# Optimization experiments

Measured on AMD Instinct MI355X. Metric: run time of the kernel, lower is better.

The kernel has to match this reference:

```python
import jax, jax.numpy as jnp
import numpy as np

N_NODES = 32  # nodes per topological level
H = 256       # hidden size
D_IN = 64     # edge feature dim
T, E = 512, 128


def _lstm_layer(x, src, dst, Wih, Whh, b, reverse):
    """One direction of one layer over the layered lattice.
    x: [T,E,Din], src/dst: [T,E] node ids in [0,N_NODES).
    Returns per-edge hidden [T,E,H].
    """
    if reverse:  # traverse lattice in reverse topological order
        x = x[::-1]
        s, d = dst[::-1], src[::-1]
    else:
        s, d = src, dst
    h0 = jnp.zeros((N_NODES, H), x.dtype)
    c0 = jnp.zeros((N_NODES, H), x.dtype)

    def step(carry, inp):
        hn, cn = carry
        xe, se, de = inp
        hs, cs = hn[se], cn[se]                      # gather source-node states [E,H]
        gates = xe @ Wih.T + hs @ Whh.T + b          # LSTMCell: [E,4H]
        i, f, g, o = jnp.split(gates, 4, axis=-1)
        c = jax.nn.sigmoid(f) * cs + jax.nn.sigmoid(i) * jnp.tanh(g)
        h = jax.nn.sigmoid(o) * jnp.tanh(c)
        # combine_edges('mean'): segment-mean of incoming edges per dest node
        cnt = jax.ops.segment_sum(jnp.ones((E,), x.dtype), de, num_segments=N_NODES)
        denom = jnp.maximum(cnt, 1.0)[:, None]
        hn2 = jax.ops.segment_sum(h, de, num_segments=N_NODES) / denom
        cn2 = jax.ops.segment_sum(c, de, num_segments=N_NODES) / denom
        return (hn2, cn2), h

    _, eh = jax.lax.scan(step, (h0, c0), (x, s, d))
    if reverse:
        eh = eh[::-1]
    return eh


def setup_inputs() -> dict:
    key = jax.random.key(0)
    ks = jax.random.split(key, 16)
    x = jax.random.normal(ks[0], (T, E, D_IN), jnp.float32)
    src = jax.random.randint(ks[1], (T, E), 0, N_NODES, jnp.int32)
    dst = jax.random.randint(ks[2], (T, E), 0, N_NODES, jnp.int32)
    sc = 1.0 / np.sqrt(H)
    u = lambda k, shp: jax.random.uniform(k, shp, jnp.float32, -sc, sc)
    # layer 0: input D_IN; layer 1: input 2H (bidirectional concat). dim 0 = direction
    W_ih0 = u(ks[3], (2, 4 * H, D_IN))
    W_hh0 = u(ks[4], (2, 4 * H, H))
    b0 = u(ks[5], (2, 4 * H))
    W_ih1 = u(ks[6], (2, 4 * H, 2 * H))
    W_hh1 = u(ks[7], (2, 4 * H, H))
    b1 = u(ks[8], (2, 4 * H))
    return {"x": x, "W_ih0": W_ih0, "W_hh0": W_hh0, "b0": b0,
            "W_ih1": W_ih1, "W_hh1": W_hh1, "b1": b1,
            "src": src, "dst": dst}


def reference(x, W_ih0, W_hh0, b0, W_ih1, W_hh1, b1, src, dst):
    out = x
    for Wih, Whh, b in ((W_ih0, W_hh0, b0), (W_ih1, W_hh1, b1)):
        fwd = _lstm_layer(out, src, dst, Wih[0], Whh[0], b[0], reverse=False)
        bwd = _lstm_layer(out, src, dst, Wih[1], Whh[1], b[1], reverse=True)
        out = jnp.concatenate([fwd, bwd], axis=-1)  # [T,E,2H]
    return out
```

## Files before the change

### kernel.cpp

```cpp
#include <hip/hip_runtime.h>

#define T_STEPS 512
#define E_EDGES 128
#define NN 32
#define HH 256
#define G4 1024
#define NWG 64
#define TPB 256

typedef __attribute__((ext_vector_type(8))) short s8v;
typedef __attribute__((ext_vector_type(4))) float f4v;
typedef unsigned long long u64;

__device__ __forceinline__ float fsig(float x) {
  x = fminf(fmaxf(x, -30.f), 30.f);
  return 1.f / (1.f + __expf(-x));
}
__device__ __forceinline__ float ftanh(float x) {
  float xc = fminf(fmaxf(x, -15.f), 15.f);
  float e = __expf(2.f * xc);
  return (e - 1.f) / (e + 1.f);
}
__device__ __forceinline__ float b2f(short s) {
  return __uint_as_float(((unsigned)(unsigned short)s) << 16);
}
__device__ __forceinline__ void bar_lds() {
  asm volatile("s_waitcnt lgkmcnt(0)\n\ts_barrier" ::: "memory");
}

__global__ __launch_bounds__(128) void prep_kernel(const int* __restrict__ src,
    const int* __restrict__ dst, int* __restrict__ eord, int* __restrict__ eoff) {
  __shared__ int de0[E_EDGES], de1[E_EDGES], off0[NN + 1], off1[NN + 1];
  const int t = blockIdx.x, e = threadIdx.x;
  de0[e] = dst[t * E_EDGES + e];
  de1[e] = src[t * E_EDGES + e];
  __syncthreads();
  if (e == 0) {
    int c[NN];
    for (int i = 0; i < NN; ++i) c[i] = 0;
    for (int i = 0; i < E_EDGES; ++i) c[de0[i]]++;
    int s = 0;
    for (int i = 0; i < NN; ++i) { off0[i] = s; s += c[i]; }
    off0[NN] = E_EDGES;
  }
  if (e == 1) {
    int c[NN];
    for (int i = 0; i < NN; ++i) c[i] = 0;
    for (int i = 0; i < E_EDGES; ++i) c[de1[i]]++;
    int s = 0;
    for (int i = 0; i < NN; ++i) { off1[i] = s; s += c[i]; }
    off1[NN] = E_EDGES;
  }
  __syncthreads();
  int d0 = de0[e], r0 = 0, d1 = de1[e], r1 = 0;
  for (int i = 0; i < e; ++i) {
    r0 += (de0[i] == d0);
    r1 += (de1[i] == d1);
  }
  eord[((size_t)0 * T_STEPS + t) * E_EDGES + off0[d0] + r0] = e;
  eord[((size_t)1 * T_STEPS + (T_STEPS - 1 - t)) * E_EDGES + off1[d1] + r1] = e;
  if (e < NN + 1) {
    eoff[((size_t)0 * T_STEPS + t) * (NN + 1) + e] = off0[e];
    eoff[((size_t)1 * T_STEPS + (T_STEPS - 1 - t)) * (NN + 1) + e] = off1[e];
  }
}

template <int M>
__global__ __launch_bounds__(256) void gates_mfma(
    const float* __restrict__ In, const float* __restrict__ W,
    const float* __restrict__ b, float* __restrict__ Gx, int reverse, int t0,
    int Cs) {
  __shared__ short WsT[2][128][72];
  __shared__ short XsT[2][128][72];
  __shared__ float biasL[128];
  const int tid = threadIdx.x;
  const int kb = blockIdx.x;
  const int lt = blockIdx.y;
  const int t = t0 + lt;
  const int tsrc = reverse ? (T_STEPS - 1 - t) : t;
  const float* Inb = In + (size_t)tsrc * E_EDGES * M;

  if (tid < 128) biasL[tid] = b[kb * 128 + tid];

  const int lane = tid & 63, wv = tid >> 6;
  const int ll = lane & 15, lh = lane >> 4;
  const int srow = tid >> 1, sh32 = (tid & 1) * 32;

  f4v acc[2][8];
#pragma unroll
  for (int i = 0; i < 2; ++i)
#pragma unroll
    for (int j = 0; j < 8; ++j) acc[i][j] = (f4v){0.f, 0.f, 0.f, 0.f};

  for (int mc = 0; mc < M; mc += 64) {
    __syncthreads();
    {
      const float* wr = W + (size_t)(kb * 128 + srow) * M + mc + sh32;
      const float* xr = Inb + (size_t)srow * M + mc + sh32;
#pragma unroll
      for (int i = 0; i < 8; ++i) {
        float4 a = *(const float4*)(wr + i * 4);
        float4 x = *(const float4*)(xr + i * 4);
        unsigned ua[4] = {__float_as_uint(a.x), __float_as_uint(a.y),
                          __float_as_uint(a.z), __float_as_uint(a.w)};
        unsigned ux[4] = {__float_as_uint(x.x), __float_as_uint(x.y),
                          __float_as_uint(x.z), __float_as_uint(x.w)};
        unsigned la[4], lx[4];
#pragma unroll
        for (int u = 0; u < 4; ++u) {
          la[u] = __float_as_uint(__uint_as_float(ua[u]) -
                                  __uint_as_float(ua[u] & 0xFFFF0000u));
          lx[u] = __float_as_uint(__uint_as_float(ux[u]) -
                                  __uint_as_float(ux[u] & 0xFFFF0000u));
        }
        int off = sh32 + i * 4;
        *(unsigned*)&WsT[0][srow][off + 0] = (ua[0] >> 16) | (ua[1] & 0xFFFF0000u);
        *(unsigned*)&WsT[0][srow][off + 2] = (ua[2] >> 16) | (ua[3] & 0xFFFF0000u);
        *(unsigned*)&WsT[1][srow][off + 0] = (la[0] >> 16) | (la[1] & 0xFFFF0000u);
        *(unsigned*)&WsT[1][srow][off + 2] = (la[2] >> 16) | (la[3] & 0xFFFF0000u);
        *(unsigned*)&XsT[0][srow][off + 0] = (ux[0] >> 16) | (ux[1] & 0xFFFF0000u);
        *(unsigned*)&XsT[0][srow][off + 2] = (ux[2] >> 16) | (ux[3] & 0xFFFF0000u);
        *(unsigned*)&XsT[1][srow][off + 0] = (lx[0] >> 16) | (lx[1] & 0xFFFF0000u);
        *(unsigned*)&XsT[1][srow][off + 2] = (lx[2] >> 16) | (lx[3] & 0xFFFF0000u);
      }
    }
    __syncthreads();
#pragma unroll
    for (int ks = 0; ks < 2; ++ks) {
      const int mo = ks * 32 + lh * 8;
      s8v ah0 = *(const s8v*)&WsT[0][wv * 32 + ll][mo];
      s8v al0 = *(const s8v*)&WsT[1][wv * 32 + ll][mo];
      s8v ah1 = *(const s8v*)&WsT[0][wv * 32 + 16 + ll][mo];
      s8v al1 = *(const s8v*)&WsT[1][wv * 32 + 16 + ll][mo];
#pragma unroll
      for (int et = 0; et < 8; ++et) {
        s8v bh = *(const s8v*)&XsT[0][et * 16 + ll][mo];
        s8v blo = *(const s8v*)&XsT[1][et * 16 + ll][mo];
        acc[0][et] = __builtin_amdgcn_mfma_f32_16x16x32_bf16(ah0, bh, acc[0][et], 0, 0, 0);
        acc[0][et] = __builtin_amdgcn_mfma_f32_16x16x32_bf16(ah0, blo, acc[0][et], 0, 0, 0);
        acc[0][et] = __builtin_amdgcn_mfma_f32_16x16x32_bf16(al0, bh, acc[0][et], 0, 0, 0);
        acc[1][et] = __builtin_amdgcn_mfma_f32_16x16x32_bf16(ah1, bh, acc[1][et], 0, 0, 0);
        acc[1][et] = __builtin_amdgcn_mfma_f32_16x16x32_bf16(ah1, blo, acc[1][et], 0, 0, 0);
        acc[1][et] = __builtin_amdgcn_mfma_f32_16x16x32_bf16(al1, bh, acc[1][et], 0, 0, 0);
      }
    }
  }
#pragma unroll
  for (int kt = 0; kt < 2; ++kt) {
    const int kloc = wv * 32 + kt * 16 + lh * 4;
    const int kg = kb * 128 + kloc;
    const int gate = kg >> 8;
    const int ch = kg & 255;
    const int slot = ch >> 3;
    const int jj0 = ch & 7;
    const float4 bv = *(const float4*)&biasL[kloc];
    float* gb = Gx + ((((size_t)slot * Cs + lt) * 4 + gate) * E_EDGES) * 8 + jj0;
#pragma unroll
    for (int et = 0; et < 8; ++et) {
      int e = et * 16 + ll;
      f4v v = acc[kt][et];
      *(float4*)(gb + (size_t)e * 8) =
          make_float4(v[0] + bv.x, v[1] + bv.y, v[2] + bv.z, v[3] + bv.w);
    }
  }
}

__global__ __launch_bounds__(TPB) void recur_kernel(
    const float* __restrict__ GxF, const float* __restrict__ GxB,
    const float* __restrict__ WhhF, const float* __restrict__ WhhB,
    const int* __restrict__ src, const int* __restrict__ dst,
    const int* __restrict__ eord, const int* __restrict__ eoff,
    u64* hnG, float* cnG, float* outBase,
    int t0, int nsteps) {
  __shared__ short WsB[2][32][33][8];
  __shared__ short hnB[2][32][33][8];
  __shared__ float zF[32][33];
  __shared__ float hE[E_EDGES][8];
  __shared__ float cE[E_EDGES][8];
  __shared__ float cnL[NN][9];
  __shared__ int eordL[E_EDGES];
  __shared__ int eoffL[NN + 1];
  __shared__ int mfmaOK;

  const int tid = threadIdx.x;
  const int wg = blockIdx.x;
  const int dir = wg >> 5;
  const int slot = wg & 31;
  const int j0 = slot * 8;
  const float* Gx = dir ? GxB : GxF;
  const float* Whh = dir ? WhhB : WhhF;
  const int* seA = dir ? dst : src;
  float* cnGd = cnG + (size_t)dir * NN * HH;

  {
    int gc = tid >> 3;
    int g = gc >> 3, jj2 = gc & 7;
    const float* wr = Whh + ((size_t)(g * HH) + j0 + jj2) * HH;
    int c0 = (tid & 7) * 32;
    for (int kk = 0; kk < 32; ++kk) {
      int k = c0 + kk;
      float f = wr[k];
      unsigned fb = __float_as_uint(f);
      unsigned hb = fb & 0xFFFF0000u;
      float lof = f - __uint_as_float(hb);
      WsB[0][k >> 3][gc][k & 7] = (short)(hb >> 16);
      WsB[1][k >> 3][gc][k & 7] = (short)(__float_as_uint(lof) >> 16);
    }
  }
  {
    int n = tid >> 3, jj = tid & 7;
    cnL[n][jj] = cnGd[n * HH + j0 + jj];
  }
  if (tid < 64) {
    s8v ta, tb;
    const int rr = tid & 15, kh = (tid >> 4) * 8;
#pragma unroll
    for (int i = 0; i < 8; ++i) {
      int k = kh + i;
      ta[i] = (short)(__float_as_uint((float)((rr + 2 * k) & 7)) >> 16);
      tb[i] = (short)(__float_as_uint((float)(((3 * k + rr) & 7) - 3)) >> 16);
    }
    f4v tacc = {0.f, 0.f, 0.f, 0.f};
    tacc = __builtin_amdgcn_mfma_f32_16x16x32_bf16(ta, tb, tacc, 0, 0, 0);
    bool ok = true;
    const int col = tid & 15, rbase = (tid >> 4) * 4;
#pragma unroll
    for (int g2 = 0; g2 < 4; ++g2) {
      int row = rbase + g2;
      float ex = 0.f;
      for (int k = 0; k < 32; ++k)
        ex += (float)((row + 2 * k) & 7) * (float)(((3 * k + col) & 7) - 3);
      ok &= (tacc[g2] == ex);
    }
    unsigned long long bb = __ballot(ok);
    if (tid == 0) mfmaOK = (bb == 0xFFFFFFFFFFFFFFFFull) ? 1 : 0;
  }
  __syncthreads();
  const bool useMfma = (mfmaOK != 0);

  const int e = tid >> 1, jh = tid & 1;
  const float* gxWG = Gx + (size_t)slot * nsteps * 4096 + (e * 8 + jh * 4);

  for (int rl = 0; rl < nsteps; ++rl) {
    const int r = t0 + rl;
    const int tv = dir ? (T_STEPS - 1 - r) : r;

    const int sec = seA[tv * E_EDGES + e];
    int eoV = 0, eofV = 0;
    if (tid < E_EDGES) eoV = eord[((size_t)dir * T_STEPS + r) * E_EDGES + tid];
    else if (tid < E_EDGES + NN + 1)
      eofV = eoff[((size_t)dir * T_STEPS + r) * (NN + 1) + (tid - E_EDGES)];
    const float* gp = gxWG + (size_t)rl * 4096;
    float4 gxi = *(const float4*)(gp + 0 * 1024);
    float4 gxf = *(const float4*)(gp + 1 * 1024);
    float4 gxg = *(const float4*)(gp + 2 * 1024);
    float4 gxo = *(const float4*)(gp + 3 * 1024);

    {
      const u64* hnRd = hnG + (size_t)((r & 1) * 2 + dir) * NN * HH;
      const unsigned want = (unsigned)(t0 + rl);
      u64 va[16], vb[16];
#pragma unroll
      for (int p = 0; p < 16; ++p) {
        int idx = tid + 256 * p;
        const u64* ptr = hnRd + (size_t)(idx >> 7) * HH + (idx & 127) * 2;
        va[p] = __hip_atomic_load(ptr, __ATOMIC_RELAXED, __HIP_MEMORY_SCOPE_AGENT);
        vb[p] = __hip_atomic_load(ptr + 1, __ATOMIC_RELAXED, __HIP_MEMORY_SCOPE_AGENT);
      }
      unsigned pend = 0xFFFFu;
      int guard = 0;
      for (;;) {
#pragma unroll
        for (int p = 0; p < 16; ++p) {
          if (pend & (1u << p)) {
            if ((unsigned)(va[p] >> 32) == want && (unsigned)(vb[p] >> 32) == want) {
              pend &= ~(1u << p);
              int idx = tid + 256 * p;
              int n = idx >> 7, c2 = idx & 127;
              unsigned u0 = (unsigned)va[p], u1 = (unsigned)vb[p];
              unsigned h0 = u0 & 0xFFFF0000u, h1 = u1 & 0xFFFF0000u;
              float l0f = __uint_as_float(u0) - __uint_as_float(h0);
              float l1f = __uint_as_float(u1) - __uint_as_float(h1);
              unsigned hw = h1 | (u0 >> 16);
              unsigned lw = (__float_as_uint(l1f) & 0xFFFF0000u) |
                            (__float_as_uint(l0f) >> 16);
              int k = c2 * 2;
              ((unsigned*)&hnB[0][k >> 3][n][0])[(k & 7) >> 1] = hw;
              ((unsigned*)&hnB[1][k >> 3][n][0])[(k & 7) >> 1] = lw;
            }
          }
        }
        if (!pend) break;
        if (++guard > (1 << 20)) break;
        __builtin_amdgcn_s_sleep(0);
#pragma unroll
        for (int p = 0; p < 16; ++p) {
          if (pend & (1u << p)) {
            int idx = tid + 256 * p;
            const u64* ptr = hnRd + (size_t)(idx >> 7) * HH + (idx & 127) * 2;
            va[p] = __hip_atomic_load(ptr, __ATOMIC_RELAXED, __HIP_MEMORY_SCOPE_AGENT);
            vb[p] = __hip_atomic_load(ptr + 1, __ATOMIC_RELAXED, __HIP_MEMORY_SCOPE_AGENT);
          }
        }
      }
      if (tid < E_EDGES) eordL[tid] = eoV;
      else if (tid < E_EDGES + NN + 1) eoffL[tid - E_EDGES] = eofV;
    }
    bar_lds();

    if (useMfma) {
      const int lane = tid & 63, wv = tid >> 6;
      const int gr = (wv >> 1) * 16;
      const int ncb = (wv & 1) * 16;
      const int ll = lane & 15, lh = lane >> 4;
      f4v ah = {0.f, 0.f, 0.f, 0.f}, bl = {0.f, 0.f, 0.f, 0.f};
#pragma unroll
      for (int kb = 0; kb < 8; ++kb) {
        s8v wh = *(const s8v*)&WsB[0][kb * 4 + lh][gr + ll][0];
        s8v wl = *(const s8v*)&WsB[1][kb * 4 + lh][gr + ll][0];
        s8v hh = *(const s8v*)&hnB[0][kb * 4 + lh][ncb + ll][0];
        s8v hl = *(const s8v*)&hnB[1][kb * 4 + lh][ncb + ll][0];
        ah = __builtin_amdgcn_mfma_f32_16x16x32_bf16(wh, hh, ah, 0, 0, 0);
        bl = __builtin_amdgcn_mfma_f32_16x16x32_bf16(wh, hl, bl, 0, 0, 0);
        bl = __builtin_amdgcn_mfma_f32_16x16x32_bf16(wl, hh, bl, 0, 0, 0);
      }
#pragma unroll
      for (int g2 = 0; g2 < 4; ++g2)
        zF[gr + lh * 4 + g2][ncb + ll] = ah[g2] + bl[g2];
    } else {
      int n = tid & 31, gq = tid >> 5;
      float za[4] = {0.f, 0.f, 0.f, 0.f};
      for (int k = 0; k < 256; ++k) {
        int kb8 = k >> 3, el = k & 7;
        float hv = b2f(hnB[0][kb8][n][el]) + b2f(hnB[1][kb8][n][el]);
#pragma unroll
        for (int q = 0; q < 4; ++q) {
          int gc = gq * 4 + q;
          za[q] += (b2f(WsB[0][kb8][gc][el]) + b2f(WsB[1][kb8][gc][el])) * hv;
        }
      }
#pragma unroll
      for (int q = 0; q < 4; ++q) zF[gq * 4 + q][n] = za[q];
    }
    bar_lds();

    {
      const float gi4[4] = {gxi.x, gxi.y, gxi.z, gxi.w};
      const float gf4[4] = {gxf.x, gxf.y, gxf.z, gxf.w};
      const float gg4[4] = {gxg.x, gxg.y, gxg.z, gxg.w};
      const float go4[4] = {gxo.x, gxo.y, gxo.z, gxo.w};
      float hq[4], cq[4];
#pragma unroll
      for (int u = 0; u < 4; ++u) {
        int jj = jh * 4 + u;
        float gi = gi4[u] + zF[jj][sec];
        float gf = gf4[u] + zF[8 + jj][sec];
        float gv = gg4[u] + zF[16 + jj][sec];
        float go = go4[u] + zF[24 + jj][sec];
        float cv = fsig(gf) * cnL[sec][jj] + fsig(gi) * ftanh(gv);
        float hv = fsig(go) * ftanh(cv);
        hq[u] = hv;
        cq[u] = cv;
      }
      *(float4*)&hE[e][jh * 4] = make_float4(hq[0], hq[1], hq[2], hq[3]);
      *(float4*)&cE[e][jh * 4] = make_float4(cq[0], cq[1], cq[2], cq[3]);
      int tw = dir ? (T_STEPS - 1 - r) : r;
      *(float4*)(outBase + ((size_t)tw * E_EDGES + e) * 512 + dir * 256 + j0 + jh * 4)
          = make_float4(hq[0], hq[1], hq[2], hq[3]);
    }
    bar_lds();

    {
      int n = tid >> 3, jj = tid & 7;
      int o0 = eoffL[n], o1 = eoffL[n + 1];
      float sh = 0.f, sc = 0.f;
      for (int o = o0; o < o1; ++o) {
        int ee = eordL[o];
        sh += hE[ee][jj];
        sc += cE[ee][jj];
      }
      int len = o1 - o0;
      float rdn = (len > 0) ? (1.f / (float)len) : 1.f;
      float hnv = sh * rdn;
      u64 pk = ((u64)(unsigned)(t0 + rl + 1) << 32) |
               (u64)__float_as_uint(hnv);
      u64* hnWr = hnG + (size_t)(((r + 1) & 1) * 2 + dir) * NN * HH +
                  (size_t)n * HH + j0 + jj;
      __hip_atomic_store(hnWr, pk, __ATOMIC_RELAXED, __HIP_MEMORY_SCOPE_AGENT);
      cnL[n][jj] = sc * rdn;
    }
    bar_lds();
  }

  {
    int n = tid >> 3, jj = tid & 7;
    cnGd[n * HH + j0 + jj] = cnL[n][jj];
  }
}

extern "C" void kernel_launch(void* const* d_in, const int* in_sizes, int n_in,
                              void* d_out, int out_size, void* d_ws, size_t ws_size,
                              hipStream_t stream) {
  const float* x = (const float*)d_in[0];
  const float* Wih0 = (const float*)d_in[1];
  const float* Whh0 = (const float*)d_in[2];
  const float* b0 = (const float*)d_in[3];
  const float* Wih1 = (const float*)d_in[4];
  const float* Whh1 = (const float*)d_in[5];
  const float* b1 = (const float*)d_in[6];
  const int* src = (const int*)d_in[7];
  const int* dst = (const int*)d_in[8];
  float* out = (float*)d_out;

  const size_t outElems = (size_t)T_STEPS * E_EDGES * 512;
  const size_t hnW = (size_t)4 * NN * HH;
  const size_t eordW = (size_t)2 * T_STEPS * E_EDGES;
  const size_t eoffW = (size_t)2 * T_STEPS * (NN + 1);
  int C = 512;
  while (C >= 1) {
    size_t need = (2 * (size_t)C * G4 * E_EDGES + outElems + 2 * hnW +
                   2 * (size_t)NN * HH + eordW + eoffW + 256) * sizeof(float);
    if (need <= ws_size) break;
    C >>= 1;
  }
  if (C < 1) return;

  float* GxF = (float*)d_ws;
  float* GxB = GxF + (size_t)C * G4 * E_EDGES;
  float* out0 = GxB + (size_t)C * G4 * E_EDGES;
  u64* hnG = (u64*)(out0 + outElems);
  float* cnG = (float*)(hnG + hnW);
  int* eord = (int*)(cnG + 2 * NN * HH);
  int* eoff = eord + eordW;

  prep_kernel<<<dim3(T_STEPS), 128, 0, stream>>>(src, dst, eord, eoff);

  for (int layer = 0; layer < 2; ++layer) {
    const float* Wih = layer ? Wih1 : Wih0;
    const float* Whh = layer ? Whh1 : Whh0;
    const float* bb = layer ? b1 : b0;
    const float* In = layer ? out0 : x;
    float* outT = layer ? out : out0;
    (void)hipMemsetAsync(hnG, 0, hnW * sizeof(u64), stream);
    (void)hipMemsetAsync(cnG, 0, 2 * NN * HH * sizeof(float), stream);
    for (int t0 = 0; t0 < T_STEPS; t0 += C) {
      if (layer == 0) {
        gates_mfma<64><<<dim3(8, C), 256, 0, stream>>>(In, Wih, bb, GxF, 0, t0, C);
        gates_mfma<64><<<dim3(8, C), 256, 0, stream>>>(In, Wih + (size_t)G4 * 64, bb + G4, GxB, 1, t0, C);
      } else {
        gates_mfma<512><<<dim3(8, C), 256, 0, stream>>>(In, Wih, bb, GxF, 0, t0, C);
        gates_mfma<512><<<dim3(8, C), 256, 0, stream>>>(In, Wih + (size_t)G4 * 512, bb + G4, GxB, 1, t0, C);
      }
      const float* gxF = GxF; const float* gxB = GxB;
      const float* whF = Whh; const float* whB = Whh + (size_t)G4 * HH;
      const int* psrc = src; const int* pdst = dst;
      const int* peord = eord; const int* peoff = eoff;
      u64* phn = hnG; float* pcn = cnG; float* pout = outT;
      int a_t0 = t0, a_ns = C;
      void* args[13] = {&gxF, &gxB, &whF, &whB, &psrc, &pdst, &peord, &peoff,
                        &phn, &pcn, &pout, &a_t0, &a_ns};
      hipLaunchCooperativeKernel((const void*)recur_kernel, dim3(NWG), dim3(TPB),
                                 args, 0, stream);
    }
  }
}
```

Measured before the change: 7.507 ms.

## Double-buffer LDS scratch to drop per-step barrier; pre-split bf16 hi/lo at producer

Double-buffers the per-step edge hidden/cell scratch and edge-order tables in LDS by step parity, so the third workgroup barrier at the end of each recurrent step can be removed. The producer now packs the hidden value into a bf16 hi/lo pair before publishing, so consumers only shuffle bits while waiting on the spin loop instead of doing float subtraction. This shortens the critical serial path per timestep, at the cost of more LDS and relying on the next step's barrier ordering for cnL reuse.

```diff
diff --git a/kernel.cpp b/kernel.cpp
--- a/kernel.cpp
+++ b/kernel.cpp
@@ -175,11 +175,11 @@
   __shared__ short WsB[2][32][33][8];
   __shared__ short hnB[2][32][33][8];
   __shared__ float zF[32][33];
-  __shared__ float hE[E_EDGES][8];
-  __shared__ float cE[E_EDGES][8];
+  __shared__ float hE[2][E_EDGES][8];
+  __shared__ float cE[2][E_EDGES][8];
   __shared__ float cnL[NN][9];
-  __shared__ int eordL[E_EDGES];
-  __shared__ int eoffL[NN + 1];
+  __shared__ int eordL[2][E_EDGES];
+  __shared__ int eoffL[2][NN + 1];
   __shared__ int mfmaOK;
 
   const int tid = threadIdx.x;
@@ -244,6 +244,7 @@
   for (int rl = 0; rl < nsteps; ++rl) {
     const int r = t0 + rl;
     const int tv = dir ? (T_STEPS - 1 - r) : r;
+    const int par = rl & 1;
 
     const int sec = seA[tv * E_EDGES + e];
     int eoV = 0, eofV = 0;
@@ -277,13 +278,10 @@
               pend &= ~(1u << p);
               int idx = tid + 256 * p;
               int n = idx >> 7, c2 = idx & 127;
-              unsigned u0 = (unsigned)va[p], u1 = (unsigned)vb[p];
-              unsigned h0 = u0 & 0xFFFF0000u, h1 = u1 & 0xFFFF0000u;
-              float l0f = __uint_as_float(u0) - __uint_as_float(h0);
-              float l1f = __uint_as_float(u1) - __uint_as_float(h1);
-              unsigned hw = h1 | (u0 >> 16);
-              unsigned lw = (__float_as_uint(l1f) & 0xFFFF0000u) |
-                            (__float_as_uint(l0f) >> 16);
+              unsigned pa = (unsigned)va[p];
+              unsigned pb = (unsigned)vb[p];
+              unsigned hw = (pa >> 16) | (pb & 0xFFFF0000u);
+              unsigned lw = (pa & 0xFFFFu) | (pb << 16);
               int k = c2 * 2;
               ((unsigned*)&hnB[0][k >> 3][n][0])[(k & 7) >> 1] = hw;
               ((unsigned*)&hnB[1][k >> 3][n][0])[(k & 7) >> 1] = lw;
@@ -303,8 +301,8 @@
           }
         }
       }
-      if (tid < E_EDGES) eordL[tid] = eoV;
-      else if (tid < E_EDGES + NN + 1) eoffL[tid - E_EDGES] = eofV;
+      if (tid < E_EDGES) eordL[par][tid] = eoV;
+      else if (tid < E_EDGES + NN + 1) eoffL[par][tid - E_EDGES] = eofV;
     }
     bar_lds();
 
@@ -362,8 +360,8 @@
         hq[u] = hv;
         cq[u] = cv;
       }
-      *(float4*)&hE[e][jh * 4] = make_float4(hq[0], hq[1], hq[2], hq[3]);
-      *(float4*)&cE[e][jh * 4] = make_float4(cq[0], cq[1], cq[2], cq[3]);
+      *(float4*)&hE[par][e][jh * 4] = make_float4(hq[0], hq[1], hq[2], hq[3]);
+      *(float4*)&cE[par][e][jh * 4] = make_float4(cq[0], cq[1], cq[2], cq[3]);
       int tw = dir ? (T_STEPS - 1 - r) : r;
       *(float4*)(outBase + ((size_t)tw * E_EDGES + e) * 512 + dir * 256 + j0 + jh * 4)
           = make_float4(hq[0], hq[1], hq[2], hq[3]);
@@ -372,25 +370,27 @@
 
     {
       int n = tid >> 3, jj = tid & 7;
-      int o0 = eoffL[n], o1 = eoffL[n + 1];
+      int o0 = eoffL[par][n], o1 = eoffL[par][n + 1];
       float sh = 0.f, sc = 0.f;
       for (int o = o0; o < o1; ++o) {
-        int ee = eordL[o];
-        sh += hE[ee][jj];
-        sc += cE[ee][jj];
+        int ee = eordL[par][o];
+        sh += hE[par][ee][jj];
+        sc += cE[par][ee][jj];
       }
       int len = o1 - o0;
       float rdn = (len > 0) ? (1.f / (float)len) : 1.f;
       float hnv = sh * rdn;
-      u64 pk = ((u64)(unsigned)(t0 + rl + 1) << 32) |
-               (u64)__float_as_uint(hnv);
+      unsigned hb = __float_as_uint(hnv) & 0xFFFF0000u;
+      float lof = hnv - __uint_as_float(hb);
+      unsigned payload = hb | (__float_as_uint(lof) >> 16);
+      u64 pk = ((u64)(unsigned)(t0 + rl + 1) << 32) | (u64)payload;
       u64* hnWr = hnG + (size_t)(((r + 1) & 1) * 2 + dir) * NN * HH +
                   (size_t)n * HH + j0 + jj;
       __hip_atomic_store(hnWr, pk, __ATOMIC_RELAXED, __HIP_MEMORY_SCOPE_AGENT);
       cnL[n][jj] = sc * rdn;
     }
-    bar_lds();
-  }
+  }
+  __syncthreads();
 
   {
     int n = tid >> 3, jj = tid & 7;
```

Result: slower. 7.683 ms (+2.4%).
